# Performance work log

Measured on AMD Instinct MI355X. Metric: run time of the kernel, lower is better.

Reference implementation:

```python
import jax, jax.numpy as jnp
import numpy as np

DIM = 64; PDIM = 16; HEADS = 8; WS = 10; KS = 13; NBLK = 2
B = 4; H = 200; W = 200


def conv2d(x, w, b=None, padding=0, groups=1):
    out = jax.lax.conv_general_dilated(
        x, w, (1, 1), [(padding, padding), (padding, padding)],
        dimension_numbers=('NCHW', 'OIHW', 'NCHW'), feature_group_count=groups)
    if b is not None:
        out = out + b[None, :, None, None]
    return out


def gelu(x):
    return jax.nn.gelu(x, approximate=False)  # torch default exact gelu


def layernorm_cf(x, w, b, eps=1e-6):
    # channels_first LayerNorm: normalize over channel axis (axis=1)
    mu = jnp.mean(x, axis=1, keepdims=True)
    var = jnp.mean((x - mu) ** 2, axis=1, keepdims=True)
    return (x - mu) * jax.lax.rsqrt(var + eps) * w[None, :, None, None] + b[None, :, None, None]


def conv_ffn(x, pw, pb, dw, db, aw, ab):
    x = gelu(conv2d(x, pw, pb))
    x = gelu(conv2d(x, dw, db, padding=dw.shape[-1] // 2, groups=x.shape[1])) + x
    return conv2d(x, aw, ab)


def geo_ensemble(k):
    k = jax.lax.stop_gradient(k)  # torch code uses .detach()
    kr = jnp.rot90(k, k=-1, axes=(2, 3))
    s = k + k[:, :, :, ::-1] + k[:, :, ::-1, :] + k[:, :, ::-1, ::-1]
    s = s + kr + kr[:, :, :, ::-1] + kr[:, :, ::-1, :] + kr[:, :, ::-1, ::-1]
    return s / 8.0


def rpe_bias(rpb, ws):
    idx = jnp.arange(ws * ws)
    h_, w_ = idx // ws, idx % ws
    rel_h = h_[None, :] - h_[:, None] + ws - 1  # k_h - q_h
    rel_w = w_[None, :] - w_[:, None] + ws - 1
    rel_idx = rel_h * (2 * ws - 1) + rel_w
    return rpb[:, rel_idx]  # [heads, N, N]


def window_attention(x, qw, qb, ow, ob, rpb):
    b, c, h, w = x.shape  # h, w divisible by WS
    hd, wd = h // WS, w // WS
    ch = c // HEADS
    qkv = conv2d(x, qw, qb)  # [b, 3c, h, w]
    t = qkv.reshape(b, 3, HEADS, ch, hd, WS, wd, WS)
    t = t.transpose(1, 0, 4, 6, 2, 5, 7, 3).reshape(3, b * hd * wd, HEADS, WS * WS, ch)
    q, k, v = t[0], t[1], t[2]
    bias = rpe_bias(rpb, WS)[None]  # [1, heads, N, N]
    score = jnp.einsum('whqc,whkc->whqk', q, k) / jnp.sqrt(jnp.float32(ch)) + bias
    attn = jax.nn.softmax(score, axis=-1)
    out = jnp.einsum('whqk,whkc->whqc', attn, v)
    out = out.reshape(b, hd, wd, HEADS, WS, WS, ch).transpose(0, 3, 6, 1, 4, 2, 5).reshape(b, c, h, w)
    return conv2d(out, ow, ob)


def conv_attention(x, lk, d1w, d1b, d2w, d2b):
    bs, c, h, w = x.shape
    x1, x2 = x[:, :PDIM], x[:, PDIM:]
    g = jnp.mean(x1, axis=(2, 3), keepdims=True)  # AdaptiveAvgPool2d(1)
    g = gelu(conv2d(g, d1w, d1b))
    dk = conv2d(g, d2w, d2b).reshape(bs * PDIM, 1, 3, 3)  # per-sample dw kernels
    x1d = conv2d(x1.reshape(1, bs * PDIM, h, w), dk, padding=1, groups=bs * PDIM)
    x1d = x1d.reshape(bs, PDIM, h, w)
    x1 = conv2d(x1, lk, padding=KS // 2) + x1d
    return jnp.concatenate([x1, x2], axis=1)


def _forward(x, ln_proj_w, ln_proj_b, proj_p_w, proj_p_b, proj_d_w, proj_d_b, proj_a_w, proj_a_b,
             ln_attn_w, ln_attn_b, qkv_w, qkv_b, attn_out_w, attn_out_b, rpb,
             dwcp1_w, dwcp1_b, dwcp2_w, dwcp2_b, pconv_aggr_w, pconv_aggr_b,
             ffn_p_w, ffn_p_b, ffn_d_w, ffn_d_b, ffn_a_w, ffn_a_b,
             ln_out_w, ln_out_b, conv_out_w, conv_out_b, plk_filter):
    skip = x
    x = layernorm_cf(x, ln_proj_w, ln_proj_b)
    x = conv_ffn(x, proj_p_w, proj_p_b, proj_d_w, proj_d_b, proj_a_w, proj_a_b)
    x = x + window_attention(layernorm_cf(x, ln_attn_w, ln_attn_b), qkv_w, qkv_b, attn_out_w, attn_out_b, rpb)
    lk = geo_ensemble(plk_filter)
    for i in range(NBLK):  # lns are Identity (use_ln=False)
        y = conv_ffn(x, ffn_p_w[i], ffn_p_b[i], ffn_d_w[i], ffn_d_b[i], ffn_a_w[i], ffn_a_b[i])
        y = conv_attention(y, lk, dwcp1_w[i], dwcp1_b[i], dwcp2_w[i], dwcp2_b[i])
        y = conv2d(y, pconv_aggr_w[i], pconv_aggr_b[i])
        x = x + y
    x = conv2d(layernorm_cf(x, ln_out_w, ln_out_b), conv_out_w, conv_out_b, padding=1)
    return x + skip


def setup_inputs() -> dict:
    key = jax.random.key(0)
    ks = jax.random.split(key, 20)
    def rn(i, shape, scale):
        return jax.random.normal(ks[i], shape, dtype=jnp.float32) * scale
    inp = {
        'x': rn(0, (B, DIM, H, W), 1.0),
        'ln_proj_w': jnp.ones(DIM, jnp.float32), 'ln_proj_b': jnp.zeros(DIM, jnp.float32),
        'proj_p_w': rn(1, (128, 64, 1, 1), 64 ** -0.5), 'proj_p_b': jnp.zeros(128, jnp.float32),
        'proj_d_w': rn(2, (128, 1, 3, 3), 1.0 / 3.0), 'proj_d_b': jnp.zeros(128, jnp.float32),
        'proj_a_w': rn(3, (64, 128, 1, 1), 128 ** -0.5), 'proj_a_b': jnp.zeros(64, jnp.float32),
        'ln_attn_w': jnp.ones(DIM, jnp.float32), 'ln_attn_b': jnp.zeros(DIM, jnp.float32),
        'qkv_w': rn(4, (192, 64, 1, 1), 64 ** -0.5), 'qkv_b': jnp.zeros(192, jnp.float32),
        'attn_out_w': rn(5, (64, 64, 1, 1), 64 ** -0.5), 'attn_out_b': jnp.zeros(64, jnp.float32),
        'rpb': rn(6, (HEADS, (2 * WS - 1) ** 2), 0.001),
        'dwcp1_w': rn(7, (2, 8, 16, 1, 1), 16 ** -0.5), 'dwcp1_b': jnp.zeros((2, 8), jnp.float32),
        'dwcp2_w': rn(8, (2, 144, 8, 1, 1), 0.01), 'dwcp2_b': jnp.zeros((2, 144), jnp.float32),
        'pconv_aggr_w': rn(9, (2, 64, 64, 1, 1), 64 ** -0.5), 'pconv_aggr_b': jnp.zeros((2, 64), jnp.float32),
        'ffn_p_w': rn(10, (2, 80, 64, 1, 1), 64 ** -0.5), 'ffn_p_b': jnp.zeros((2, 80), jnp.float32),
        'ffn_d_w': rn(11, (2, 80, 1, 3, 3), 1.0 / 3.0), 'ffn_d_b': jnp.zeros((2, 80), jnp.float32),
        'ffn_a_w': rn(12, (2, 64, 80, 1, 1), 80 ** -0.5), 'ffn_a_b': jnp.zeros((2, 64), jnp.float32),
        'ln_out_w': jnp.ones(DIM, jnp.float32), 'ln_out_b': jnp.zeros(DIM, jnp.float32),
        'conv_out_w': rn(13, (64, 64, 3, 3), (64 * 9) ** -0.5), 'conv_out_b': jnp.zeros(64, jnp.float32),
        'plk_filter': rn(14, (PDIM, PDIM, KS, KS), (PDIM * KS * KS) ** -0.5),
    }
    return inp


def reference(x, ln_proj_w, ln_proj_b, proj_p_w, proj_p_b, proj_d_w, proj_d_b, proj_a_w, proj_a_b,
              ln_attn_w, ln_attn_b, qkv_w, qkv_b, attn_out_w, attn_out_b, rpb,
              dwcp1_w, dwcp1_b, dwcp2_w, dwcp2_b, pconv_aggr_w, pconv_aggr_b,
              ffn_p_w, ffn_p_b, ffn_d_w, ffn_d_b, ffn_a_w, ffn_a_b,
              ln_out_w, ln_out_b, conv_out_w, conv_out_b, plk_filter):
    return _forward(x, ln_proj_w, ln_proj_b, proj_p_w, proj_p_b, proj_d_w, proj_d_b, proj_a_w, proj_a_b,
                    ln_attn_w, ln_attn_b, qkv_w, qkv_b, attn_out_w, attn_out_b, rpb,
                    dwcp1_w, dwcp1_b, dwcp2_w, dwcp2_b, pconv_aggr_w, pconv_aggr_b,
                    ffn_p_w, ffn_p_b, ffn_d_w, ffn_d_b, ffn_a_w, ffn_a_b,
                    ln_out_w, ln_out_b, conv_out_w, conv_out_b, plk_filter)
```

## Files before the change

kernel.cpp:

```cpp
#include <hip/hip_runtime.h>
#include <math.h>

#define HH 200
#define WW 200
#define HWP 40000
#define NP4 10000
#define BB 4

#define LKS 40
#define DPS 24
#define PARTSZ 2560000

typedef __fp16 f16x2 __attribute__((ext_vector_type(2)));
typedef __fp16 f16x8 __attribute__((ext_vector_type(8)));
typedef float fx4 __attribute__((ext_vector_type(4)));

#if __has_builtin(__builtin_amdgcn_fdot2)
__device__ __forceinline__ float fdot2f(f16x2 a, f16x2 b, float c) {
    return __builtin_amdgcn_fdot2(a, b, c, false);
}
#else
__device__ __forceinline__ float fdot2f(f16x2 a, f16x2 b, float c) {
    return c + (float)a[0] * (float)b[0] + (float)a[1] * (float)b[1];
}
#endif

__device__ __forceinline__ f16x2 pk2(float a, float b) {
    return __builtin_amdgcn_cvt_pkrtz(a, b);
}

__device__ __forceinline__ float gelu_f(float x) {
    return 0.5f * x * (1.0f + erff(x * 0.7071067811865475f));
}

__global__ __launch_bounds__(256) void prep_kernel(
    const float* __restrict__ pc, f16x2* __restrict__ wth)
{
    int i = blockIdx.x * 256 + threadIdx.x;
    if (i >= 4096) return;
    int w = i >> 11;
    int r = i & 2047;
    int c2 = r / 64, o = r - c2 * 64;
    const float* src = pc + w * 4096;
    f16x2 v;
    v[0] = (__fp16)src[o * 64 + 2 * c2];
    v[1] = (__fp16)src[o * 64 + 2 * c2 + 1];
    wth[w * 2048 + r] = v;
}

__global__ __launch_bounds__(256) void prepA_kernel(
    const float* __restrict__ qkvw, const float* __restrict__ pp,
    const float* __restrict__ ao, const float* __restrict__ fp,
    f16x8* __restrict__ wA)
{
    int s = blockIdx.x * 256 + threadIdx.x;
    if (s >= 4352) return;
    const float* src;
    int base;
    if (s < 1536)      { src = qkvw;      base = 0; }
    else if (s < 2560) { src = pp;        base = 1536; }
    else if (s < 3072) { src = ao;        base = 2560; }
    else if (s < 3712) { src = fp;        base = 3072; }
    else               { src = fp + 5120; base = 3712; }
    int r = s - base;
    int lane = r & 63;
    int t = r >> 6;
    int ks = t & 1;
    int cot = t >> 1;
    int co = cot * 16 + (lane & 15);
    int k0 = ks * 32 + ((lane >> 4) << 3);
    f16x8 v;
#pragma unroll
    for (int j = 0; j < 8; ++j) v[j] = (__fp16)src[co * 64 + k0 + j];
    wA[s] = v;
}

__global__ __launch_bounds__(256) void prepA2_kernel(
    const float* __restrict__ pa, const float* __restrict__ fa,
    f16x8* __restrict__ wA2)
{
    int s = blockIdx.x * 256 + threadIdx.x;
    if (s >= 2560) return;
    const float* src; int base, Ci, ksteps;
    if (s < 1024)      { src = pa;        base = 0;    Ci = 128; ksteps = 4; }
    else if (s < 1792) { src = fa;        base = 1024; Ci = 80;  ksteps = 3; }
    else               { src = fa + 5120; base = 1792; Ci = 80;  ksteps = 3; }
    int r = s - base;
    int lane = r & 63;
    int u = r >> 6;
    int ks = u % ksteps;
    int cot = u / ksteps;
    int co = cot * 16 + (lane & 15);
    int k0 = ks * 32 + ((lane >> 4) << 3);
    f16x8 v;
#pragma unroll
    for (int j = 0; j < 8; ++j) {
        int k = k0 + j;
        v[j] = (k < Ci) ? (__fp16)src[co * Ci + k] : (__fp16)0.f;
    }
    wA2[s] = v;
}

__global__ __launch_bounds__(256) void prepA3_kernel(
    const float* __restrict__ co3, f16x8* __restrict__ wA3)
{
    int s = blockIdx.x * 256 + threadIdx.x;
    if (s >= 4608) return;
    int lane = s & 63;
    int u = s >> 6;
    int cot = u & 3;
    int t = u >> 2;
    int co = cot * 16 + (lane & 15);
    int k0 = t * 32 + ((lane >> 4) << 3);
    f16x8 v;
#pragma unroll
    for (int j = 0; j < 8; ++j) {
        int k = k0 + j;
        int tap = k >> 6, ci = k & 63;
        v[j] = (__fp16)co3[(co * 64 + ci) * 9 + tap];
    }
    wA3[s] = v;
}

__global__ __launch_bounds__(256, 2) void ln_kernel(
    const float* __restrict__ in, const float* __restrict__ w,
    const float* __restrict__ b, float* __restrict__ out)
{
    int p = blockIdx.x * 256 + threadIdx.x;
    int bb = blockIdx.y;
    if (p >= HWP) return;
    const float* ib = in + (size_t)bb * 64 * HWP + p;
    float v[64];
    float mu = 0.f;
#pragma unroll
    for (int c = 0; c < 64; ++c) { v[c] = ib[(size_t)c * HWP]; mu += v[c]; }
    mu *= (1.f / 64.f);
    float var = 0.f;
#pragma unroll
    for (int c = 0; c < 64; ++c) { float d = v[c] - mu; var += d * d; }
    var *= (1.f / 64.f);
    float r = rsqrtf(var + 1e-6f);
    float* ob = out + (size_t)bb * 64 * HWP + p;
#pragma unroll
    for (int c = 0; c < 64; ++c) ob[(size_t)c * HWP] = (v[c] - mu) * r * w[c] + b[c];
}

__global__ __launch_bounds__(256, 2) void conv1x1_mfma_kernel(
    const float* __restrict__ in, const f16x8* __restrict__ wA,
    const float* __restrict__ bias, float* __restrict__ out,
    int Co, int do_gelu, int do_add)
{
    int lane = threadIdx.x & 63;
    int wv = threadIdx.x >> 6;
    int px0 = blockIdx.x * 256 + wv * 64;
    if (px0 >= HWP) return;
    int bb = blockIdx.z;
    int cot0 = blockIdx.y * 4;
    int nCot = (Co >> 4) - cot0; if (nCot > 4) nCot = 4;
    int row = lane >> 4;
    int colp = lane & 15;

    fx4 acc[4][4];
#pragma unroll
    for (int c = 0; c < 4; ++c)
#pragma unroll
        for (int nt = 0; nt < 4; ++nt)
#pragma unroll
            for (int r = 0; r < 4; ++r) acc[c][nt][r] = 0.f;

    const float* ib = in + (size_t)bb * 64 * HWP;
#pragma unroll
    for (int ks = 0; ks < 2; ++ks) {
        f16x8 afr[4];
#pragma unroll
        for (int c = 0; c < 4; ++c)
            if (c < nCot) afr[c] = wA[(((cot0 + c) * 2 + ks) << 6) + lane];
#pragma unroll
        for (int nt = 0; nt < 4; ++nt) {
            int px = px0 + nt * 16 + colp;
            const float* bp = ib + (size_t)(ks * 32 + row * 8) * HWP + px;
            union { f16x8 v; f16x2 h[4]; } bu;
            bu.h[0] = pk2(bp[0],              bp[(size_t)1 * HWP]);
            bu.h[1] = pk2(bp[(size_t)2 * HWP], bp[(size_t)3 * HWP]);
            bu.h[2] = pk2(bp[(size_t)4 * HWP], bp[(size_t)5 * HWP]);
            bu.h[3] = pk2(bp[(size_t)6 * HWP], bp[(size_t)7 * HWP]);
#pragma unroll
            for (int c = 0; c < 4; ++c)
                if (c < nCot)
                    acc[c][nt] = __builtin_amdgcn_mfma_f32_16x16x32_f16(afr[c], bu.v, acc[c][nt], 0, 0, 0);
        }
    }

#pragma unroll
    for (int c = 0; c < 4; ++c) {
        if (c < nCot) {
#pragma unroll
            for (int r = 0; r < 4; ++r) {
                int co = (cot0 + c) * 16 + row * 4 + r;
                float bv = bias[co];
                float* op = out + ((size_t)bb * Co + co) * HWP;
#pragma unroll
                for (int nt = 0; nt < 4; ++nt) {
                    int px = px0 + nt * 16 + colp;
                    float v = acc[c][nt][r] + bv;
                    if (do_gelu) v = gelu_f(v);
                    if (do_add) v += op[px];
                    op[px] = v;
                }
            }
        }
    }
}

__global__ __launch_bounds__(256, 2) void conv1x1h_mfma_kernel(
    const __fp16* __restrict__ in,
    const f16x8* __restrict__ wA,
    const float* __restrict__ bias, float* __restrict__ out,
    int Ci, int ksteps)
{
    int lane = threadIdx.x & 63;
    int wv = threadIdx.x >> 6;
    int px0 = blockIdx.x * 256 + wv * 64;
    if (px0 >= HWP) return;
    int bb = blockIdx.z;
    int row = lane >> 4;
    int colp = lane & 15;

    fx4 acc[4][4];
#pragma unroll
    for (int c = 0; c < 4; ++c)
#pragma unroll
        for (int nt = 0; nt < 4; ++nt)
#pragma unroll
            for (int r = 0; r < 4; ++r) acc[c][nt][r] = 0.f;

    const __fp16* ib = in + (size_t)bb * Ci * HWP;
    for (int ks = 0; ks < ksteps; ++ks) {
        f16x8 afr[4];
#pragma unroll
        for (int c = 0; c < 4; ++c)
            afr[c] = wA[((c * ksteps + ks) << 6) + lane];
        int k0 = ks * 32 + row * 8;
        bool ok = (k0 < Ci);
#pragma unroll
        for (int nt = 0; nt < 4; ++nt) {
            int px = px0 + nt * 16 + colp;
            f16x8 bv;
            if (ok) {
                const __fp16* bp = ib + (size_t)k0 * HWP + px;
#pragma unroll
                for (int j = 0; j < 8; ++j) bv[j] = bp[(size_t)j * HWP];
            } else {
#pragma unroll
                for (int j = 0; j < 8; ++j) bv[j] = (__fp16)0.f;
            }
#pragma unroll
            for (int c = 0; c < 4; ++c)
                acc[c][nt] = __builtin_amdgcn_mfma_f32_16x16x32_f16(afr[c], bv, acc[c][nt], 0, 0, 0);
        }
    }

#pragma unroll
    for (int c = 0; c < 4; ++c) {
#pragma unroll
        for (int r = 0; r < 4; ++r) {
            int co = c * 16 + row * 4 + r;
            float bv = bias[co];
            float* op = out + ((size_t)bb * 64 + co) * HWP;
#pragma unroll
            for (int nt = 0; nt < 4; ++nt) {
                int px = px0 + nt * 16 + colp;
                op[px] = acc[c][nt][r] + bv;
            }
        }
    }
}

__global__ __launch_bounds__(256, 2) void conv3_mfma_kernel(
    const float* __restrict__ in,
    const f16x8* __restrict__ wA3,
    const float* __restrict__ bias, const float* __restrict__ skip,
    float* __restrict__ out)
{
    int lane = threadIdx.x & 63;
    int wv = threadIdx.x >> 6;
    int px0 = blockIdx.x * 256 + wv * 64;
    if (px0 >= HWP) return;
    int bb = blockIdx.z;
    int row = lane >> 4;
    int colp = lane & 15;

    fx4 acc[4][4];
#pragma unroll
    for (int c = 0; c < 4; ++c)
#pragma unroll
        for (int nt = 0; nt < 4; ++nt)
#pragma unroll
            for (int r = 0; r < 4; ++r) acc[c][nt][r] = 0.f;

    int py[4], pxx[4];
#pragma unroll
    for (int nt = 0; nt < 4; ++nt) {
        int p = px0 + nt * 16 + colp;
        py[nt] = p / WW;
        pxx[nt] = p - py[nt] * WW;
    }

    const float* ib = in + (size_t)bb * 64 * HWP;
    for (int t = 0; t < 18; ++t) {
        int tap = t >> 1, ks = t & 1;
        int dy = tap / 3 - 1, dx = tap % 3 - 1;
        f16x8 afr[4];
#pragma unroll
        for (int c = 0; c < 4; ++c) afr[c] = wA3[((t * 4 + c) << 6) + lane];
        const float* kb = ib + (size_t)(ks * 32 + row * 8) * HWP;
#pragma unroll
        for (int nt = 0; nt < 4; ++nt) {
            int yy = py[nt] + dy, xx = pxx[nt] + dx;
            union { f16x8 v; f16x2 h[4]; } bu;
            if ((unsigned)yy < HH && (unsigned)xx < WW) {
                const float* bp = kb + yy * WW + xx;
                bu.h[0] = pk2(bp[0],              bp[(size_t)1 * HWP]);
                bu.h[1] = pk2(bp[(size_t)2 * HWP], bp[(size_t)3 * HWP]);
                bu.h[2] = pk2(bp[(size_t)4 * HWP], bp[(size_t)5 * HWP]);
                bu.h[3] = pk2(bp[(size_t)6 * HWP], bp[(size_t)7 * HWP]);
            } else {
                bu.h[0] = pk2(0.f, 0.f); bu.h[1] = bu.h[0];
                bu.h[2] = bu.h[0];       bu.h[3] = bu.h[0];
            }
#pragma unroll
            for (int c = 0; c < 4; ++c)
                acc[c][nt] = __builtin_amdgcn_mfma_f32_16x16x32_f16(afr[c], bu.v, acc[c][nt], 0, 0, 0);
        }
    }

#pragma unroll
    for (int c = 0; c < 4; ++c) {
#pragma unroll
        for (int r = 0; r < 4; ++r) {
            int co = c * 16 + row * 4 + r;
            float bv = bias[co];
            const float* sb = skip + ((size_t)bb * 64 + co) * HWP;
            float* op = out + ((size_t)bb * 64 + co) * HWP;
#pragma unroll
            for (int nt = 0; nt < 4; ++nt) {
                int px = px0 + nt * 16 + colp;
                op[px] = acc[c][nt][r] + bv + sb[px];
            }
        }
    }
}

__global__ __launch_bounds__(256, 4) void dwgelu_kernel(
    const float* __restrict__ in,
    const float* __restrict__ dw,
    const float* __restrict__ db,
    __fp16* __restrict__ vout,
    int Ci)
{
    __shared__ float s_p[16][18 * DPS];
    int tid = threadIdx.x;
    int tx = tid & 15, ty = tid >> 4;
    int x0 = blockIdx.x * 16, y0 = blockIdx.y * 16;
    int part = blockIdx.z & 3;
    int bb = blockIdx.z >> 2;
    int cic = Ci >> 2;
    int cbase = part * cic;
    int x = x0 + tx, y = y0 + ty;
    bool inb = (x < WW && y < HH);
    int p = y * WW + x;

    const float* ibase = in + (size_t)bb * Ci * HWP;
    __fp16* obase = vout + (size_t)bb * Ci * HWP;
    for (int c0 = cbase; c0 < cbase + cic; c0 += 16) {
        int chunk = cbase + cic - c0; if (chunk > 16) chunk = 16;
        __syncthreads();
        for (int i = tid; i < chunk * 324; i += 256) {
            int ci = i / 324; int r = i - ci * 324;
            int py = r / 18, px = r - py * 18;
            int yy = y0 + py - 1, xx = x0 + px - 1;
            float v = 0.f;
            if ((unsigned)yy < HH && (unsigned)xx < WW)
                v = ibase[(size_t)(c0 + ci) * HWP + yy * WW + xx];
            s_p[ci][py * DPS + px] = v;
        }
        __syncthreads();
        if (inb) {
            for (int ci = 0; ci < chunk; ++ci) {
                int c = c0 + ci;
                float s = db[c];
                const float* dwr = dw + c * 9;
#pragma unroll
                for (int ky = 0; ky < 3; ++ky)
#pragma unroll
                    for (int kx = 0; kx < 3; ++kx)
                        s += s_p[ci][(ty + ky) * DPS + tx + kx] * dwr[ky * 3 + kx];
                float v = gelu_f(s) + s_p[ci][(ty + 1) * DPS + tx + 1];
                obase[(size_t)c * HWP + p] = (__fp16)v;
            }
        }
    }
}

__global__ __launch_bounds__(128, 4) void winattn2_kernel(
    const float* __restrict__ qkv,
    const float* __restrict__ rpb,
    float* __restrict__ out)
{
    __shared__ __align__(16) f16x2 s_k2[100][4];
    __shared__ __align__(4) __fp16 s_vT[8][100];
    __shared__ float s_b[361];

    int head = blockIdx.y, bb = blockIdx.z;
    int wy = blockIdx.x / 20, wx = blockIdx.x - wy * 20;
    int tid = threadIdx.x;

    for (int i = tid; i < 361; i += 128) s_b[i] = rpb[head * 361 + i];

    int ty = tid / 10, tx = tid - ty * 10;
    f16x2 q2[4];
    if (tid < 100) {
        int y = wy * 10 + ty, x = wx * 10 + tx;
        int gp = y * WW + x;
        const float* qb = qkv + ((size_t)bb * 192 + head * 8) * HWP + gp;
        const float* kb = qb + (size_t)64 * HWP;
        const float* vb = qb + (size_t)128 * HWP;
        const float scale = 0.3535533905932738f;
#pragma unroll
        for (int c2 = 0; c2 < 4; ++c2) {
            q2[c2] = pk2(qb[(size_t)(2 * c2) * HWP] * scale,
                         qb[(size_t)(2 * c2 + 1) * HWP] * scale);
            s_k2[tid][c2] = pk2(kb[(size_t)(2 * c2) * HWP], kb[(size_t)(2 * c2 + 1) * HWP]);
        }
#pragma unroll
        for (int cc = 0; cc < 8; ++cc)
            s_vT[cc][tid] = (__fp16)vb[(size_t)cc * HWP];
    }
    __syncthreads();

    if (tid < 100) {
        const float* brow = s_b + (180 - ty * 19 - tx);

        f16x2 s16[50];
        float m = -1e30f;
#pragma unroll
        for (int i = 0; i < 50; ++i) {
            const int k0 = 2 * i, k1 = 2 * i + 1;
            const int c0 = (k0 / 10) * 19 + (k0 % 10);
            const int c1 = (k1 / 10) * 19 + (k1 % 10);
            float s0 = brow[c0];
            float s1 = brow[c1];
#pragma unroll
            for (int c2 = 0; c2 < 4; ++c2) {
                s0 = fdot2f(q2[c2], s_k2[k0][c2], s0);
                s1 = fdot2f(q2[c2], s_k2[k1][c2], s1);
            }
            m = fmaxf(m, fmaxf(s0, s1));
            s16[i] = pk2(s0, s1);
        }
        float l = 0.f;
        float o[8];
#pragma unroll
        for (int cc = 0; cc < 8; ++cc) o[cc] = 0.f;
#pragma unroll
        for (int i = 0; i < 50; ++i) {
            float e0 = __expf((float)s16[i][0] - m);
            float e1 = __expf((float)s16[i][1] - m);
            l += e0 + e1;
            f16x2 e2 = pk2(e0, e1);
#pragma unroll
            for (int cc = 0; cc < 8; ++cc)
                o[cc] = fdot2f(e2, *(const f16x2*)&s_vT[cc][2 * i], o[cc]);
        }
        float rl = 1.f / l;
        int y = wy * 10 + ty, x = wx * 10 + tx;
        float* ob = out + ((size_t)bb * 64 + head * 8) * HWP + y * WW + x;
#pragma unroll
        for (int cc = 0; cc < 8; ++cc) ob[(size_t)cc * HWP] = o[cc] * rl;
    }
}

__global__ __launch_bounds__(256) void geo_kernel(
    const float* __restrict__ k, f16x2* __restrict__ out)
{
    int i = blockIdx.x * 256 + threadIdx.x;
    if (i >= 3584) return;
    int p = i / 448;
    int r = i - p * 448;
    int rep = r >> 4, co = r & 15;
    int a = 0, rr = rep;
    while (rr >= 7 - a) { rr -= 7 - a; ++a; }
    int b2 = a + rr;
    int y = 6 + a, x = 6 + b2;
    float sv[2];
#pragma unroll
    for (int t = 0; t < 2; ++t) {
        int ci = 2 * p + t;
        const float* kb = k + (co * 16 + ci) * 169;
        float s = kb[y * 13 + x] + kb[y * 13 + (12 - x)] + kb[(12 - y) * 13 + x] + kb[(12 - y) * 13 + (12 - x)]
                + kb[(12 - x) * 13 + y] + kb[x * 13 + y] + kb[(12 - x) * 13 + (12 - y)] + kb[x * 13 + (12 - y)];
        sv[t] = s * 0.125f;
    }
    f16x2 v;
    v[0] = (__fp16)sv[0];
    v[1] = (__fp16)sv[1];
    out[i] = v;
}

__global__ __launch_bounds__(256) void gmean_kernel(
    const float* __restrict__ in, float* __restrict__ g)
{
    int bc = blockIdx.x;
    int bb = bc >> 4, c = bc & 15;
    const float* p = in + ((size_t)bb * 64 + c) * HWP;
    float s = 0.f;
    for (int i = threadIdx.x; i < HWP; i += 256) s += p[i];
#pragma unroll
    for (int off = 32; off > 0; off >>= 1) s += __shfl_down(s, off);
    __shared__ float red[4];
    int wave = threadIdx.x >> 6;
    if ((threadIdx.x & 63) == 0) red[wave] = s;
    __syncthreads();
    if (threadIdx.x == 0)
        g[bc] = (red[0] + red[1] + red[2] + red[3]) * (1.f / 40000.f);
}

__global__ __launch_bounds__(192) void dynk_kernel(
    const float* __restrict__ g, const float* __restrict__ w1, const float* __restrict__ b1,
    const float* __restrict__ w2, const float* __restrict__ b2, float* __restrict__ dk)
{
    int bb = blockIdx.x;
    __shared__ float s_g2[8];
    int tid = threadIdx.x;
    if (tid < 8) {
        float a = b1[tid];
        for (int c = 0; c < 16; ++c) a += w1[tid * 16 + c] * g[bb * 16 + c];
        s_g2[tid] = gelu_f(a);
    }
    __syncthreads();
    if (tid < 144) {
        float a = b2[tid];
#pragma unroll
        for (int i = 0; i < 8; ++i) a += w2[tid * 8 + i] * s_g2[i];
        dk[bb * 144 + tid] = a;
    }
}

__global__ __launch_bounds__(256, 6) void lkconv_kernel(
    const float* __restrict__ in,
    const f16x2* __restrict__ lkP,
    const float* __restrict__ dk,
    float* __restrict__ out)
{
    __shared__ f16x2 s_p[2][28 * LKS];
    int z = blockIdx.z;
    int bb = z >> 2, q = z & 3;
    int tid = threadIdx.x;
    int tx = tid & 15, ty = tid >> 4;
    int x0 = blockIdx.x * 16, y0 = blockIdx.y * 16;
    int x = x0 + tx, y = y0 + ty;

    const float* ib = in + ((size_t)bb * 64 + q * 4) * HWP;
    for (int i = tid; i < 2 * 784; i += 256) {
        int pi = i / 784; int r = i - pi * 784;
        int py = r / 28, px = r - py * 28;
        int yy = y0 + py - 6, xx = x0 + px - 6;
        f16x2 v = pk2(0.f, 0.f);
        if ((unsigned)yy < HH && (unsigned)xx < WW) {
            int gp = yy * WW + xx;
            v = pk2(ib[(size_t)(2 * pi) * HWP + gp], ib[(size_t)(2 * pi + 1) * HWP + gp]);
        }
        s_p[pi][py * LKS + px] = v;
    }
    __syncthreads();

    float acc[16];
#pragma unroll
    for (int co = 0; co < 16; ++co) acc[co] = 0.f;

#pragma unroll
    for (int pi = 0; pi < 2; ++pi) {
        f16x2 orb[28];
#pragma unroll
        for (int o = 0; o < 28; ++o) orb[o] = pk2(0.f, 0.f);
#pragma unroll
        for (int ky = 0; ky < 13; ++ky) {
#pragma unroll
            for (int kx = 0; kx < 13; ++kx) {
                const int a = (ky < 6) ? (6 - ky) : (ky - 6);
                const int b = (kx < 6) ? (6 - kx) : (kx - 6);
                const int lo = (a < b) ? a : b;
                const int hi = (a < b) ? b : a;
                const int idx = lo * 7 - (lo * (lo - 1)) / 2 + (hi - lo);
                orb[idx] += s_p[pi][(ty + ky) * LKS + tx + kx];
            }
        }
        const f16x2* wci = lkP + (size_t)(q * 2 + pi) * 28 * 16;
#pragma unroll
        for (int o = 0; o < 28; ++o) {
            f16x2 ov = orb[o];
            const f16x2* wr = wci + o * 16;
#pragma unroll
            for (int co = 0; co < 16; ++co) acc[co] = fdot2f(ov, wr[co], acc[co]);
        }
#pragma unroll
        for (int h = 0; h < 2; ++h) {
            int ci = q * 4 + 2 * pi + h;
            float d = 0.f;
            const float* dkr = dk + bb * 144 + ci * 9;
#pragma unroll
            for (int dy = 0; dy < 3; ++dy)
#pragma unroll
                for (int dx = 0; dx < 3; ++dx)
                    d += (float)s_p[pi][(ty + 5 + dy) * LKS + tx + 5 + dx][h] * dkr[dy * 3 + dx];
#pragma unroll
            for (int co = 0; co < 16; ++co) acc[co] += (co == ci) ? d : 0.f;
        }
    }

    if (x < WW && y < HH) {
        int p = y * WW + x;
        float* ob = out + (size_t)q * PARTSZ + (size_t)bb * 16 * HWP + p;
#pragma unroll
        for (int co = 0; co < 16; ++co) ob[(size_t)co * HWP] = acc[co];
    }
}

__global__ __launch_bounds__(256, 2) void pconv_add_kernel(
    const float* __restrict__ x1q,
    const float* __restrict__ yy,
    const f16x2* __restrict__ wt,
    const float* __restrict__ bias,
    float* __restrict__ xout)
{
    int p4 = blockIdx.x * 256 + threadIdx.x;
    int o0 = blockIdx.y * 16;
    int bb = blockIdx.z;
    if (p4 >= NP4) return;
    float4 acc[16];
#pragma unroll
    for (int j = 0; j < 16; ++j) {
        float bv = bias[o0 + j];
        acc[j] = make_float4(bv, bv, bv, bv);
    }
    const float4* xb0 = (const float4*)(x1q + (size_t)bb * 16 * HWP) + p4;
    const float4* xb1 = (const float4*)(x1q + PARTSZ + (size_t)bb * 16 * HWP) + p4;
    const float4* xb2 = (const float4*)(x1q + 2 * PARTSZ + (size_t)bb * 16 * HWP) + p4;
    const float4* xb3 = (const float4*)(x1q + 3 * PARTSZ + (size_t)bb * 16 * HWP) + p4;
    for (int c2 = 0; c2 < 8; ++c2) {
        int ca = 2 * c2, cb = 2 * c2 + 1;
        float4 a0 = xb0[(size_t)ca * NP4], a1 = xb1[(size_t)ca * NP4];
        float4 a2 = xb2[(size_t)ca * NP4], a3 = xb3[(size_t)ca * NP4];
        float4 s0;
        s0.x = (a0.x + a1.x) + (a2.x + a3.x);
        s0.y = (a0.y + a1.y) + (a2.y + a3.y);
        s0.z = (a0.z + a1.z) + (a2.z + a3.z);
        s0.w = (a0.w + a1.w) + (a2.w + a3.w);
        a0 = xb0[(size_t)cb * NP4]; a1 = xb1[(size_t)cb * NP4];
        a2 = xb2[(size_t)cb * NP4]; a3 = xb3[(size_t)cb * NP4];
        float4 s1;
        s1.x = (a0.x + a1.x) + (a2.x + a3.x);
        s1.y = (a0.y + a1.y) + (a2.y + a3.y);
        s1.z = (a0.z + a1.z) + (a2.z + a3.z);
        s1.w = (a0.w + a1.w) + (a2.w + a3.w);
        f16x2 px = pk2(s0.x, s1.x), py = pk2(s0.y, s1.y);
        f16x2 pz = pk2(s0.z, s1.z), pw = pk2(s0.w, s1.w);
        const f16x2* wr = wt + c2 * 64 + o0;
#pragma unroll
        for (int j = 0; j < 16; ++j) {
            f16x2 w = wr[j];
            acc[j].x = fdot2f(px, w, acc[j].x);
            acc[j].y = fdot2f(py, w, acc[j].y);
            acc[j].z = fdot2f(pz, w, acc[j].z);
            acc[j].w = fdot2f(pw, w, acc[j].w);
        }
    }
    const float4* yb = (const float4*)(yy + ((size_t)bb * 64 + 16) * HWP) + p4;
    for (int c2 = 8; c2 < 32; ++c2) {
        int cy = 2 * (c2 - 8);
        float4 s0 = yb[(size_t)cy * NP4];
        float4 s1 = yb[(size_t)(cy + 1) * NP4];
        f16x2 px = pk2(s0.x, s1.x), py = pk2(s0.y, s1.y);
        f16x2 pz = pk2(s0.z, s1.z), pw = pk2(s0.w, s1.w);
        const f16x2* wr = wt + c2 * 64 + o0;
#pragma unroll
        for (int j = 0; j < 16; ++j) {
            f16x2 w = wr[j];
            acc[j].x = fdot2f(px, w, acc[j].x);
            acc[j].y = fdot2f(py, w, acc[j].y);
            acc[j].z = fdot2f(pz, w, acc[j].z);
            acc[j].w = fdot2f(pw, w, acc[j].w);
        }
    }
    float4* ob = (float4*)(xout + ((size_t)bb * 64 + o0) * HWP) + p4;
#pragma unroll
    for (int j = 0; j < 16; ++j) {
        float4 old = ob[(size_t)j * NP4];
        old.x += acc[j].x; old.y += acc[j].y; old.z += acc[j].z; old.w += acc[j].w;
        ob[(size_t)j * NP4] = old;
    }
}

extern "C" void kernel_launch(void* const* d_in, const int* in_sizes, int n_in,
                              void* d_out, int out_size, void* d_ws, size_t ws_size,
                              hipStream_t stream)
{
    const float* x_in      = (const float*)d_in[0];
    const float* ln_proj_w = (const float*)d_in[1];
    const float* ln_proj_b = (const float*)d_in[2];
    const float* proj_p_w  = (const float*)d_in[3];
    const float* proj_p_b  = (const float*)d_in[4];
    const float* proj_d_w  = (const float*)d_in[5];
    const float* proj_d_b  = (const float*)d_in[6];
    const float* proj_a_w  = (const float*)d_in[7];
    const float* proj_a_b  = (const float*)d_in[8];
    const float* ln_attn_w = (const float*)d_in[9];
    const float* ln_attn_b = (const float*)d_in[10];
    const float* qkv_w     = (const float*)d_in[11];
    const float* qkv_b     = (const float*)d_in[12];
    const float* attn_o_w  = (const float*)d_in[13];
    const float* attn_o_b  = (const float*)d_in[14];
    const float* rpb       = (const float*)d_in[15];
    const float* dwcp1_w   = (const float*)d_in[16];
    const float* dwcp1_b   = (const float*)d_in[17];
    const float* dwcp2_w   = (const float*)d_in[18];
    const float* dwcp2_b   = (const float*)d_in[19];
    const float* pconv_w   = (const float*)d_in[20];
    const float* pconv_b   = (const float*)d_in[21];
    const float* ffn_p_w   = (const float*)d_in[22];
    const float* ffn_p_b   = (const float*)d_in[23];
    const float* ffn_d_w   = (const float*)d_in[24];
    const float* ffn_d_b   = (const float*)d_in[25];
    const float* ffn_a_w   = (const float*)d_in[26];
    const float* ffn_a_b   = (const float*)d_in[27];
    const float* ln_out_w  = (const float*)d_in[28];
    const float* ln_out_b  = (const float*)d_in[29];
    const float* conv_o_w  = (const float*)d_in[30];
    const float* conv_o_b  = (const float*)d_in[31];
    const float* plk       = (const float*)d_in[32];

    float* X  = (float*)d_out;
    float* ws = (float*)d_ws;

    float* A    = ws;
    float* Y    = ws;
    float* R1   = ws + 10240000;
    float* QKV  = ws + 10240000;
    __fp16* Vf  = (__fp16*)(ws + 23040000);
    __fp16* Vp  = (__fp16*)(ws + 30720000);
    float* R2Q  = ws + 33280000;
    f16x2* LKTH = (f16x2*)(ws + 43520000);
    float* GM   = ws + 43524096;
    float* DK   = GM + 64;
    f16x2* WTH  = (f16x2*)(DK + 576);
    f16x8* WAH  = (f16x8*)(DK + 576 + 4096);
    f16x8* WA2  = WAH + 4352;
    f16x8* WA3  = WA2 + 2560;

    dim3 b256(256);
    dim3 gLN(157, 4);
    dim3 gT16(13, 13, 16);
    dim3 gM1(157, 1, 4);

    prep_kernel<<<dim3(16), b256, 0, stream>>>(pconv_w, WTH);
    prepA_kernel<<<dim3(17), b256, 0, stream>>>(qkv_w, proj_p_w, attn_o_w, ffn_p_w, WAH);
    prepA2_kernel<<<dim3(10), b256, 0, stream>>>(proj_a_w, ffn_a_w, WA2);
    prepA3_kernel<<<dim3(18), b256, 0, stream>>>(conv_o_w, WA3);
    geo_kernel<<<dim3(14), b256, 0, stream>>>(plk, LKTH);

    ln_kernel<<<gLN, b256, 0, stream>>>(x_in, ln_proj_w, ln_proj_b, A);
    conv1x1_mfma_kernel<<<dim3(157, 2, 4), b256, 0, stream>>>(A, WAH + 1536, proj_p_b, R1, 128, 1, 0);
    dwgelu_kernel<<<gT16, b256, 0, stream>>>(R1, proj_d_w, proj_d_b, Vp, 128);
    conv1x1h_mfma_kernel<<<gM1, b256, 0, stream>>>(Vp, WA2 + 0, proj_a_b, X, 128, 4);

    ln_kernel<<<gLN, b256, 0, stream>>>(X, ln_attn_w, ln_attn_b, A);
    conv1x1_mfma_kernel<<<dim3(157, 3, 4), b256, 0, stream>>>(A, WAH + 0, qkv_b, QKV, 192, 0, 0);
    winattn2_kernel<<<dim3(400, 8, 4), dim3(128), 0, stream>>>(QKV, rpb, A);
    conv1x1_mfma_kernel<<<gM1, b256, 0, stream>>>(A, WAH + 2560, attn_o_b, X, 64, 0, 1);

    for (int i = 0; i < 2; ++i) {
        conv1x1_mfma_kernel<<<dim3(157, 2, 4), b256, 0, stream>>>(X, WAH + 3072 + i * 640, ffn_p_b + i * 80, R1, 80, 1, 0);
        dwgelu_kernel<<<gT16, b256, 0, stream>>>(R1, ffn_d_w + i * 720, ffn_d_b + i * 80, Vf, 80);
        conv1x1h_mfma_kernel<<<gM1, b256, 0, stream>>>(Vf, WA2 + 1024 + i * 768, ffn_a_b + i * 64, Y, 80, 3);
        gmean_kernel<<<dim3(64), b256, 0, stream>>>(Y, GM);
        dynk_kernel<<<dim3(4), dim3(192), 0, stream>>>(GM, dwcp1_w + i * 128, dwcp1_b + i * 8,
                                                       dwcp2_w + i * 1152, dwcp2_b + i * 144, DK);
        lkconv_kernel<<<gT16, b256, 0, stream>>>(Y, LKTH, DK, R2Q);
        pconv_add_kernel<<<dim3(40, 4, 4), b256, 0, stream>>>(R2Q, Y, WTH + i * 2048, pconv_b + i * 64, X);
    }

    ln_kernel<<<gLN, b256, 0, stream>>>(X, ln_out_w, ln_out_b, A);
    conv3_mfma_kernel<<<gM1, b256, 0, stream>>>(A, WA3, conv_o_b, x_in, X);
}
```

Measured before the change: 947.1 us.

## Store intermediate activations in fp16 across LN, conv and attention stages

Intermediate buffers (layernorm outputs, the pointwise-conv outputs feeding the depthwise conv, QKV, and attention outputs) are now stored as fp16 instead of fp32. The conv kernel is generalized to read fp16 input with a configurable Co, gelu and add. Consumers (dwgelu, window attention, conv3) read fp16 directly. Softmax switches to exp2 with log2e folded into the scale and bias. This roughly halves the memory traffic of these bandwidth-bound stages, at the cost of some extra rounding on the activations.

```diff
diff --git a/kernel.cpp b/kernel.cpp
--- a/kernel.cpp
+++ b/kernel.cpp
@@ -124,7 +124,7 @@
 
 __global__ __launch_bounds__(256, 2) void ln_kernel(
     const float* __restrict__ in, const float* __restrict__ w,
-    const float* __restrict__ b, float* __restrict__ out)
+    const float* __restrict__ b, __fp16* __restrict__ out)
 {
     int p = blockIdx.x * 256 + threadIdx.x;
     int bb = blockIdx.y;
@@ -140,14 +140,14 @@
     for (int c = 0; c < 64; ++c) { float d = v[c] - mu; var += d * d; }
     var *= (1.f / 64.f);
     float r = rsqrtf(var + 1e-6f);
-    float* ob = out + (size_t)bb * 64 * HWP + p;
-#pragma unroll
-    for (int c = 0; c < 64; ++c) ob[(size_t)c * HWP] = (v[c] - mu) * r * w[c] + b[c];
+    __fp16* ob = out + (size_t)bb * 64 * HWP + p;
+#pragma unroll
+    for (int c = 0; c < 64; ++c) ob[(size_t)c * HWP] = (__fp16)((v[c] - mu) * r * w[c] + b[c]);
 }
 
 __global__ __launch_bounds__(256, 2) void conv1x1_mfma_kernel(
     const float* __restrict__ in, const f16x8* __restrict__ wA,
-    const float* __restrict__ bias, float* __restrict__ out,
+    const float* __restrict__ bias, float* outf, __fp16* outh,
     int Co, int do_gelu, int do_add)
 {
     int lane = threadIdx.x & 63;
@@ -198,25 +198,105 @@
             for (int r = 0; r < 4; ++r) {
                 int co = (cot0 + c) * 16 + row * 4 + r;
                 float bv = bias[co];
-                float* op = out + ((size_t)bb * Co + co) * HWP;
 #pragma unroll
                 for (int nt = 0; nt < 4; ++nt) {
                     int px = px0 + nt * 16 + colp;
                     float v = acc[c][nt][r] + bv;
                     if (do_gelu) v = gelu_f(v);
-                    if (do_add) v += op[px];
-                    op[px] = v;
+                    if (outh) {
+                        outh[((size_t)bb * Co + co) * HWP + px] = (__fp16)v;
+                    } else {
+                        float* op = outf + ((size_t)bb * Co + co) * HWP;
+                        if (do_add) v += op[px];
+                        op[px] = v;
+                    }
                 }
             }
         }
     }
 }
 
-__global__ __launch_bounds__(256, 2) void conv1x1h_mfma_kernel(
+__global__ __launch_bounds__(256, 2) void convh_kernel(
     const __fp16* __restrict__ in,
     const f16x8* __restrict__ wA,
-    const float* __restrict__ bias, float* __restrict__ out,
-    int Ci, int ksteps)
+    const float* __restrict__ bias, float* outf, __fp16* outh,
+    int Ci, int ksteps, int Co, int do_gelu, int do_add)
+{
+    int lane = threadIdx.x & 63;
+    int wv = threadIdx.x >> 6;
+    int px0 = blockIdx.x * 256 + wv * 64;
+    if (px0 >= HWP) return;
+    int bb = blockIdx.z;
+    int cot0 = blockIdx.y * 4;
+    int nCot = (Co >> 4) - cot0; if (nCot > 4) nCot = 4;
+    int row = lane >> 4;
+    int colp = lane & 15;
+
+    fx4 acc[4][4];
+#pragma unroll
+    for (int c = 0; c < 4; ++c)
+#pragma unroll
+        for (int nt = 0; nt < 4; ++nt)
+#pragma unroll
+            for (int r = 0; r < 4; ++r) acc[c][nt][r] = 0.f;
+
+    const __fp16* ib = in + (size_t)bb * Ci * HWP;
+    for (int ks = 0; ks < ksteps; ++ks) {
+        f16x8 afr[4];
+#pragma unroll
+        for (int c = 0; c < 4; ++c)
+            if (c < nCot) afr[c] = wA[(((cot0 + c) * ksteps + ks) << 6) + lane];
+        int k0 = ks * 32 + row * 8;
+        bool ok = (k0 < Ci);
+#pragma unroll
+        for (int nt = 0; nt < 4; ++nt) {
+            int px = px0 + nt * 16 + colp;
+            f16x8 bv;
+            if (ok) {
+                const __fp16* bp = ib + (size_t)k0 * HWP + px;
+#pragma unroll
+                for (int j = 0; j < 8; ++j) bv[j] = bp[(size_t)j * HWP];
+            } else {
+#pragma unroll
+                for (int j = 0; j < 8; ++j) bv[j] = (__fp16)0.f;
+            }
+#pragma unroll
+            for (int c = 0; c < 4; ++c)
+                if (c < nCot)
+                    acc[c][nt] = __builtin_amdgcn_mfma_f32_16x16x32_f16(afr[c], bv, acc[c][nt], 0, 0, 0);
+        }
+    }
+
+#pragma unroll
+    for (int c = 0; c < 4; ++c) {
+        if (c < nCot) {
+#pragma unroll
+            for (int r = 0; r < 4; ++r) {
+                int co = (cot0 + c) * 16 + row * 4 + r;
+                float bv = bias[co];
+#pragma unroll
+                for (int nt = 0; nt < 4; ++nt) {
+                    int px = px0 + nt * 16 + colp;
+                    float v = acc[c][nt][r] + bv;
+                    if (do_gelu) v = gelu_f(v);
+                    if (outh) {
+                        outh[((size_t)bb * Co + co) * HWP + px] = (__fp16)v;
+                    } else {
+                        float* op = outf + ((size_t)bb * Co + co) * HWP;
+                        if (do_add) v += op[px];
+                        op[px] = v;
+                    }
+                }
+            }
+        }
+    }
+}
+
+__global__ __launch_bounds__(256, 2) void conv3_mfma_kernel(
+    const __fp16* __restrict__ in,
+    const f16x8* __restrict__ wA3,
+    const float* __restrict__ bias, const float* __restrict__ skip,
+    float* __restrict__ out)
 {
     int lane = threadIdx.x & 63;
     int wv = threadIdx.x >> 6;
@@ -234,70 +314,6 @@
 #pragma unroll
             for (int r = 0; r < 4; ++r) acc[c][nt][r] = 0.f;
 
-    const __fp16* ib = in + (size_t)bb * Ci * HWP;
-    for (int ks = 0; ks < ksteps; ++ks) {
-        f16x8 afr[4];
-#pragma unroll
-        for (int c = 0; c < 4; ++c)
-            afr[c] = wA[((c * ksteps + ks) << 6) + lane];
-        int k0 = ks * 32 + row * 8;
-        bool ok = (k0 < Ci);
-#pragma unroll
-        for (int nt = 0; nt < 4; ++nt) {
-            int px = px0 + nt * 16 + colp;
-            f16x8 bv;
-            if (ok) {
-                const __fp16* bp = ib + (size_t)k0 * HWP + px;
-#pragma unroll
-                for (int j = 0; j < 8; ++j) bv[j] = bp[(size_t)j * HWP];
-            } else {
-#pragma unroll
-                for (int j = 0; j < 8; ++j) bv[j] = (__fp16)0.f;
-            }
-#pragma unroll
-            for (int c = 0; c < 4; ++c)
-                acc[c][nt] = __builtin_amdgcn_mfma_f32_16x16x32_f16(afr[c], bv, acc[c][nt], 0, 0, 0);
-        }
-    }
-
-#pragma unroll
-    for (int c = 0; c < 4; ++c) {
-#pragma unroll
-        for (int r = 0; r < 4; ++r) {
-            int co = c * 16 + row * 4 + r;
-            float bv = bias[co];
-            float* op = out + ((size_t)bb * 64 + co) * HWP;
-#pragma unroll
-            for (int nt = 0; nt < 4; ++nt) {
-                int px = px0 + nt * 16 + colp;
-                op[px] = acc[c][nt][r] + bv;
-            }
-        }
-    }
-}
-
-__global__ __launch_bounds__(256, 2) void conv3_mfma_kernel(
-    const float* __restrict__ in,
-    const f16x8* __restrict__ wA3,
-    const float* __restrict__ bias, const float* __restrict__ skip,
-    float* __restrict__ out)
-{
-    int lane = threadIdx.x & 63;
-    int wv = threadIdx.x >> 6;
-    int px0 = blockIdx.x * 256 + wv * 64;
-    if (px0 >= HWP) return;
-    int bb = blockIdx.z;
-    int row = lane >> 4;
-    int colp = lane & 15;
-
-    fx4 acc[4][4];
-#pragma unroll
-    for (int c = 0; c < 4; ++c)
-#pragma unroll
-        for (int nt = 0; nt < 4; ++nt)
-#pragma unroll
-            for (int r = 0; r < 4; ++r) acc[c][nt][r] = 0.f;
-
     int py[4], pxx[4];
 #pragma unroll
     for (int nt = 0; nt < 4; ++nt) {
@@ -306,31 +322,29 @@
         pxx[nt] = p - py[nt] * WW;
     }
 
-    const float* ib = in + (size_t)bb * 64 * HWP;
+    const __fp16* ib = in + (size_t)bb * 64 * HWP;
     for (int t = 0; t < 18; ++t) {
         int tap = t >> 1, ks = t & 1;
         int dy = tap / 3 - 1, dx = tap % 3 - 1;
         f16x8 afr[4];
 #pragma unroll
         for (int c = 0; c < 4; ++c) afr[c] = wA3[((t * 4 + c) << 6) + lane];
-        const float* kb = ib + (size_t)(ks * 32 + row * 8) * HWP;
+        const __fp16* kb = ib + (size_t)(ks * 32 + row * 8) * HWP;
 #pragma unroll
         for (int nt = 0; nt < 4; ++nt) {
             int yy = py[nt] + dy, xx = pxx[nt] + dx;
-            union { f16x8 v; f16x2 h[4]; } bu;
+            f16x8 bv;
             if ((unsigned)yy < HH && (unsigned)xx < WW) {
-                const float* bp = kb + yy * WW + xx;
-                bu.h[0] = pk2(bp[0],              bp[(size_t)1 * HWP]);
-                bu.h[1] = pk2(bp[(size_t)2 * HWP], bp[(size_t)3 * HWP]);
-                bu.h[2] = pk2(bp[(size_t)4 * HWP], bp[(size_t)5 * HWP]);
-                bu.h[3] = pk2(bp[(size_t)6 * HWP], bp[(size_t)7 * HWP]);
+                const __fp16* bp = kb + yy * WW + xx;
+#pragma unroll
+                for (int j = 0; j < 8; ++j) bv[j] = bp[(size_t)j * HWP];
             } else {
-                bu.h[0] = pk2(0.f, 0.f); bu.h[1] = bu.h[0];
-                bu.h[2] = bu.h[0];       bu.h[3] = bu.h[0];
+#pragma unroll
+                for (int j = 0; j < 8; ++j) bv[j] = (__fp16)0.f;
             }
 #pragma unroll
             for (int c = 0; c < 4; ++c)
-                acc[c][nt] = __builtin_amdgcn_mfma_f32_16x16x32_f16(afr[c], bu.v, acc[c][nt], 0, 0, 0);
+                acc[c][nt] = __builtin_amdgcn_mfma_f32_16x16x32_f16(afr[c], bv, acc[c][nt], 0, 0, 0);
         }
     }
 
@@ -352,7 +366,7 @@
 }
 
 __global__ __launch_bounds__(256, 4) void dwgelu_kernel(
-    const float* __restrict__ in,
+    const __fp16* __restrict__ in,
     const float* __restrict__ dw,
     const float* __restrict__ db,
     __fp16* __restrict__ vout,
@@ -370,7 +384,7 @@
     bool inb = (x < WW && y < HH);
     int p = y * WW + x;
 
-    const float* ibase = in + (size_t)bb * Ci * HWP;
+    const __fp16* ibase = in + (size_t)bb * Ci * HWP;
     __fp16* obase = vout + (size_t)bb * Ci * HWP;
     for (int c0 = cbase; c0 < cbase + cic; c0 += 16) {
         int chunk = cbase + cic - c0; if (chunk > 16) chunk = 16;
@@ -381,7 +395,7 @@
             int yy = y0 + py - 1, xx = x0 + px - 1;
             float v = 0.f;
             if ((unsigned)yy < HH && (unsigned)xx < WW)
-                v = ibase[(size_t)(c0 + ci) * HWP + yy * WW + xx];
+                v = (float)ibase[(size_t)(c0 + ci) * HWP + yy * WW + xx];
             s_p[ci][py * DPS + px] = v;
         }
         __syncthreads();
@@ -403,9 +417,9 @@
 }
 
 __global__ __launch_bounds__(128, 4) void winattn2_kernel(
-    const float* __restrict__ qkv,
+    const __fp16* __restrict__ qkv,
     const float* __restrict__ rpb,
-    float* __restrict__ out)
+    __fp16* __restrict__ out)
 {
     __shared__ __align__(16) f16x2 s_k2[100][4];
     __shared__ __align__(4) __fp16 s_vT[8][100];
@@ -415,26 +429,30 @@
     int wy = blockIdx.x / 20, wx = blockIdx.x - wy * 20;
     int tid = threadIdx.x;
 
-    for (int i = tid; i < 361; i += 128) s_b[i] = rpb[head * 361 + i];
+    const float log2e = 1.4426950408889634f;
+    for (int i = tid; i < 361; i += 128) s_b[i] = rpb[head * 361 + i] * log2e;
 
     int ty = tid / 10, tx = tid - ty * 10;
     f16x2 q2[4];
     if (tid < 100) {
         int y = wy * 10 + ty, x = wx * 10 + tx;
         int gp = y * WW + x;
-        const float* qb = qkv + ((size_t)bb * 192 + head * 8) * HWP + gp;
-        const float* kb = qb + (size_t)64 * HWP;
-        const float* vb = qb + (size_t)128 * HWP;
-        const float scale = 0.3535533905932738f;
+        const __fp16* qb = qkv + ((size_t)bb * 192 + head * 8) * HWP + gp;
+        const __fp16* kb = qb + (size_t)64 * HWP;
+        const __fp16* vb = qb + (size_t)128 * HWP;
+        const float qsc = 0.3535533905932738f * log2e;
 #pragma unroll
         for (int c2 = 0; c2 < 4; ++c2) {
-            q2[c2] = pk2(qb[(size_t)(2 * c2) * HWP] * scale,
-                         qb[(size_t)(2 * c2 + 1) * HWP] * scale);
-            s_k2[tid][c2] = pk2(kb[(size_t)(2 * c2) * HWP], kb[(size_t)(2 * c2 + 1) * HWP]);
+            q2[c2] = pk2((float)qb[(size_t)(2 * c2) * HWP] * qsc,
+                         (float)qb[(size_t)(2 * c2 + 1) * HWP] * qsc);
+            f16x2 kv;
+            kv[0] = kb[(size_t)(2 * c2) * HWP];
+            kv[1] = kb[(size_t)(2 * c2 + 1) * HWP];
+            s_k2[tid][c2] = kv;
         }
 #pragma unroll
         for (int cc = 0; cc < 8; ++cc)
-            s_vT[cc][tid] = (__fp16)vb[(size_t)cc * HWP];
+            s_vT[cc][tid] = vb[(size_t)cc * HWP];
     }
     __syncthreads();
 
@@ -464,8 +482,8 @@
         for (int cc = 0; cc < 8; ++cc) o[cc] = 0.f;
 #pragma unroll
         for (int i = 0; i < 50; ++i) {
-            float e0 = __expf((float)s16[i][0] - m);
-            float e1 = __expf((float)s16[i][1] - m);
+            float e0 = exp2f((float)s16[i][0] - m);
+            float e1 = exp2f((float)s16[i][1] - m);
             l += e0 + e1;
             f16x2 e2 = pk2(e0, e1);
 #pragma unroll
@@ -474,9 +492,9 @@
         }
         float rl = 1.f / l;
         int y = wy * 10 + ty, x = wx * 10 + tx;
-        float* ob = out + ((size_t)bb * 64 + head * 8) * HWP + y * WW + x;
-#pragma unroll
-        for (int cc = 0; cc < 8; ++cc) ob[(size_t)cc * HWP] = o[cc] * rl;
+        __fp16* ob = out + ((size_t)bb * 64 + head * 8) * HWP + y * WW + x;
+#pragma unroll
+        for (int cc = 0; cc < 8; ++cc) ob[(size_t)cc * HWP] = (__fp16)(o[cc] * rl);
     }
 }
 
@@ -742,13 +760,12 @@
     float* X  = (float*)d_out;
     float* ws = (float*)d_ws;
 
-    float* A    = ws;
-    float* Y    = ws;
-    float* R1   = ws + 10240000;
-    float* QKV  = ws + 10240000;
-    __fp16* Vf  = (__fp16*)(ws + 23040000);
-    __fp16* Vp  = (__fp16*)(ws + 30720000);
-    float* R2Q  = ws + 33280000;
+    float*  Y    = ws;
+    __fp16* A16  = (__fp16*)ws;
+    __fp16* R1h  = (__fp16*)(ws + 10240000);
+    __fp16* QKVh = (__fp16*)(ws + 10240000);
+    __fp16* Vh   = (__fp16*)(ws + 23040000);
+    float*  R2Q  = ws + 33280000;
     f16x2* LKTH = (f16x2*)(ws + 43520000);
     float* GM   = ws + 43524096;
     float* DK   = GM + 64;
@@ -760,7 +777,6 @@
     dim3 b256(256);
     dim3 gLN(157, 4);
     dim3 gT16(13, 13, 16);
-    dim3 gM1(157, 1, 4);
 
     prep_kernel<<<dim3(16), b256, 0, stream>>>(pconv_w, WTH);
     prepA_kernel<<<dim3(17), b256, 0, stream>>>(qkv_w, proj_p_w, attn_o_w, ffn_p_w, WAH);
@@ -768,20 +784,26 @@
     prepA3_kernel<<<dim3(18), b256, 0, stream>>>(conv_o_w, WA3);
     geo_kernel<<<dim3(14), b256, 0, stream>>>(plk, LKTH);
 
-    ln_kernel<<<gLN, b256, 0, stream>>>(x_in, ln_proj_w, ln_proj_b, A);
-    conv1x1_mfma_kernel<<<dim3(157, 2, 4), b256, 0, stream>>>(A, WAH + 1536, proj_p_b, R1, 128, 1, 0);
-    dwgelu_kernel<<<gT16, b256, 0, stream>>>(R1, proj_d_w, proj_d_b, Vp, 128);
-    conv1x1h_mfma_kernel<<<gM1, b256, 0, stream>>>(Vp, WA2 + 0, proj_a_b, X, 128, 4);
-
-    ln_kernel<<<gLN, b256, 0, stream>>>(X, ln_attn_w, ln_attn_b, A);
-    conv1x1_mfma_kernel<<<dim3(157, 3, 4), b256, 0, stream>>>(A, WAH + 0, qkv_b, QKV, 192, 0, 0);
-    winattn2_kernel<<<dim3(400, 8, 4), dim3(128), 0, stream>>>(QKV, rpb, A);
-    conv1x1_mfma_kernel<<<gM1, b256, 0, stream>>>(A, WAH + 2560, attn_o_b, X, 64, 0, 1);
+    ln_kernel<<<gLN, b256, 0, stream>>>(x_in, ln_proj_w, ln_proj_b, A16);
+    convh_kernel<<<dim3(157, 2, 4), b256, 0, stream>>>(A16, WAH + 1536, proj_p_b,
+                                                       nullptr, R1h, 64, 2, 128, 1, 0);
+    dwgelu_kernel<<<gT16, b256, 0, stream>>>(R1h, proj_d_w, proj_d_b, Vh, 128);
+    convh_kernel<<<dim3(157, 1, 4), b256, 0, stream>>>(Vh, WA2 + 0, proj_a_b,
+                                                       X, nullptr, 128, 4, 64, 0, 0);
+
+    ln_kernel<<<gLN, b256, 0, stream>>>(X, ln_attn_w, ln_attn_b, A16);
+    convh_kernel<<<dim3(157, 3, 4), b256, 0, stream>>>(A16, WAH + 0, qkv_b,
+                                                       nullptr, QKVh, 64, 2, 192, 0, 0);
+    winattn2_kernel<<<dim3(400, 8, 4), dim3(128), 0, stream>>>(QKVh, rpb, A16);
+    convh_kernel<<<dim3(157, 1, 4), b256, 0, stream>>>(A16, WAH + 2560, attn_o_b,
+                                                       X, nullptr, 64, 2, 64, 0, 1);
 
     for (int i = 0; i < 2; ++i) {
-        conv1x1_mfma_kernel<<<dim3(157, 2, 4), b256, 0, stream>>>(X, WAH + 3072 + i * 640, ffn_p_b + i * 80, R1, 80, 1, 0);
-        dwgelu_kernel<<<gT16, b256, 0, stream>>>(R1, ffn_d_w + i * 720, ffn_d_b + i * 80, Vf, 80);
-        conv1x1h_mfma_kernel<<<gM1, b256, 0, stream>>>(Vf, WA2 + 1024 + i * 768, ffn_a_b + i * 64, Y, 80, 3);
+        conv1x1_mfma_kernel<<<dim3(157, 2, 4), b256, 0, stream>>>(X, WAH + 3072 + i * 640,
+                                                                  ffn_p_b + i * 80, nullptr, R1h, 80, 1, 0);
+        dwgelu_kernel<<<gT16, b256, 0, stream>>>(R1h, ffn_d_w + i * 720, ffn_d_b + i * 80, Vh, 80);
+        convh_kernel<<<dim3(157, 1, 4), b256, 0, stream>>>(Vh, WA2 + 1024 + i * 768,
+                                                           ffn_a_b + i * 64, Y, nullptr, 80, 3, 64, 0, 0);
         gmean_kernel<<<dim3(64), b256, 0, stream>>>(Y, GM);
         dynk_kernel<<<dim3(4), dim3(192), 0, stream>>>(GM, dwcp1_w + i * 128, dwcp1_b + i * 8,
                                                        dwcp2_w + i * 1152, dwcp2_b + i * 144, DK);
@@ -789,6 +811,6 @@
         pconv_add_kernel<<<dim3(40, 4, 4), b256, 0, stream>>>(R2Q, Y, WTH + i * 2048, pconv_b + i * 64, X);
     }
 
-    ln_kernel<<<gLN, b256, 0, stream>>>(X, ln_out_w, ln_out_b, A);
-    conv3_mfma_kernel<<<gM1, b256, 0, stream>>>(A, WA3, conv_o_b, x_in, X);
-}
+    ln_kernel<<<gLN, b256, 0, stream>>>(X, ln_out_w, ln_out_b, A16);
+    conv3_mfma_kernel<<<dim3(157, 1, 4), b256, 0, stream>>>(A16, WA3, conv_o_b, x_in, X);
+}
```

After: 939.2 us. No clear change (-0.8%).
